# Performance work log

Hardware: AMD Instinct MI355X
Metric: run time of the kernel (lower is better)

## Reference

```python
import jax, jax.numpy as jnp
import numpy as np

T, B, D, H, V = 48, 512, 1024, 1024, 8


def setup_inputs() -> dict:
    key = jax.random.key(0)
    k = jax.random.split(key, 8)
    s = 1.0 / np.sqrt(H)  # torch default LSTM init scale
    return {
        "decoder_hiddens": jax.random.normal(k[0], (T, 1, B, D), dtype=jnp.float32),
        "outputs": jax.random.normal(k[1], (T, B, V), dtype=jnp.float32),
        "captions": jax.random.randint(k[2], (T, B), 0, 10000, dtype=jnp.int64),
        "W_ih": jax.random.uniform(k[3], (4 * H, 2 * D), jnp.float32, -s, s),
        "W_hh": jax.random.uniform(k[4], (4 * H, H), jnp.float32, -s, s),
        "b_ih": jax.random.uniform(k[5], (4 * H,), jnp.float32, -s, s),
        "b_hh": jax.random.uniform(k[6], (4 * H,), jnp.float32, -s, s),
    }


def reference(decoder_hiddens, outputs, captions, W_ih, W_hh, b_ih, b_hh):
    # decoder_hiddens: [T, 1, B, D] -> [T, B, D] (num_layers*dirs flattened into D)
    dh = decoder_hiddens.transpose(0, 2, 1, 3).reshape(T, B, -1)

    # caption mask: tokens != 0 (pad) and != 2 (EOS)
    mask = ((captions != 0) & (captions != 2)).astype(dh.dtype)  # [T, B]
    lens = mask.sum(axis=0)  # [B]
    pooled = (mask[:, :, None] * dh).sum(axis=0) / lens[:, None]  # [B, D]

    # per-step input: cat([decoder_hidden_t, pooled]) for t = 1..T-1
    xs = jnp.concatenate(
        [dh[1:], jnp.broadcast_to(pooled, (T - 1, B, dh.shape[-1]))], axis=-1
    )  # [T-1, B, 2D]

    def lstm_step(carry, x):
        h, c = carry
        gates = x @ W_ih.T + b_ih + h @ W_hh.T + b_hh  # [B, 4H]
        i, f, g, o = jnp.split(gates, 4, axis=-1)  # torch gate order i,f,g,o
        i, f, o = jax.nn.sigmoid(i), jax.nn.sigmoid(f), jax.nn.sigmoid(o)
        c = f * c + i * jnp.tanh(g)
        h = o * jnp.tanh(c)
        return (h, c), h

    h0 = jnp.zeros((B, H), dh.dtype)
    c0 = jnp.zeros((B, H), dh.dtype)
    _, hs = jax.lax.scan(lstm_step, (h0, c0), xs)  # [T-1, B, H]

    # feats_recons[0] stays zero (loop starts at t=1), then transpose to [B, T, H]
    feats = jnp.concatenate([jnp.zeros((1, B, H), dh.dtype), hs], axis=0)
    return feats.transpose(1, 0, 2)
```

## Files before the change

kernel.cpp:

```cpp
#include <hip/hip_runtime.h>
#include <math.h>
#include <stdint.h>

#define B_ 512
#define D_ 1024
#define H_ 1024
#define T_ 48
#define NG 4096

typedef _Float16 half8 __attribute__((ext_vector_type(8)));
typedef float f32x4 __attribute__((ext_vector_type(4)));

#define AG_LOAD(p)      __hip_atomic_load((p), __ATOMIC_RELAXED, __HIP_MEMORY_SCOPE_AGENT)
#define AG_STORE(p, v)  __hip_atomic_store((p), (v), __ATOMIC_RELAXED, __HIP_MEMORY_SCOPE_AGENT)

__device__ __forceinline__ void cp16(const void* g, void* l) {
  __builtin_amdgcn_global_load_lds(
      (__attribute__((address_space(1))) const unsigned int*)(uintptr_t)g,
      (__attribute__((address_space(3))) unsigned int*)(uintptr_t)l, 16, 0, 0);
}

__device__ __forceinline__ float sigmoidf_(float x) { return 1.0f / (1.0f + expf(-x)); }

__device__ __forceinline__ float fast_sig(float x) {
  return __builtin_amdgcn_rcpf(1.0f + __expf(-x));
}
__device__ __forceinline__ float fast_tanh(float x) {
  return 1.0f - 2.0f * __builtin_amdgcn_rcpf(1.0f + __expf(2.0f * x));
}

__global__ void prep_w(const float* __restrict__ W_ih,
                       _Float16* __restrict__ Wx1, _Float16* __restrict__ Wp) {
  int idx = blockIdx.x * 256 + threadIdx.x;
  const int n1 = NG * H_;
  if (idx < n1) {
    int j = idx >> 10, k = idx & 1023;
    Wx1[idx] = (_Float16)W_ih[j * 2048 + k];
  } else {
    int i3 = idx - n1;
    int j = i3 >> 10, k = i3 & 1023;
    Wp[i3] = (_Float16)W_ih[j * 2048 + 1024 + k];
  }
}

__global__ void prep_wfrag(const float* __restrict__ W_hh, _Float16* __restrict__ Wf) {
  int f = blockIdx.x * 256 + threadIdx.x;
  int cb = f >> 13;
  int rem = f & 8191;
  int n = rem >> 11;
  int kc = (rem >> 6) & 31;
  int lane = rem & 63;
  int l16 = lane & 15, quad = lane >> 4;
  const float* s = W_hh + (size_t)(n * 1024 + cb * 16 + l16) * 1024 + kc * 32 + quad * 8;
  half8 v;
#pragma unroll
  for (int i = 0; i < 8; ++i) v[i] = (_Float16)s[i];
  *(half8*)(Wf + (size_t)f * 8) = v;
}

__global__ void pool_conv(const float* __restrict__ dh, const int* __restrict__ caps,
                          _Float16* __restrict__ dh16, _Float16* __restrict__ pooled16) {
  int tid = blockIdx.x * 256 + threadIdx.x;
  int b = tid >> 10;
  float sum = 0.0f, cnt = 0.0f;
  for (int t = 0; t < T_; ++t) {
    int cap = caps[t * B_ + b];
    float v = dh[(size_t)t * (B_ * D_) + tid];
    if (cap != 0 && cap != 2) { sum += v; cnt += 1.0f; }
    if (t >= 1) dh16[(size_t)t * (B_ * D_) + tid] = (_Float16)v;
  }
  pooled16[tid] = (_Float16)(sum / cnt);
}

__global__ void init_zero(float* __restrict__ out, unsigned* __restrict__ bar) {
  int tid = blockIdx.x * 256 + threadIdx.x;
  int b = tid >> 10, d = tid & 1023;
  out[(size_t)b * (T_ * H_) + d] = 0.0f;
  if (tid < 4096) AG_STORE(&bar[tid], 0u);
}

__global__ __launch_bounds__(256) void gemm_pool(
    const _Float16* __restrict__ A, const _Float16* __restrict__ Wp,
    const float* __restrict__ b_ih, const float* __restrict__ b_hh,
    float* __restrict__ Xc) {
  __shared__ __align__(16) _Float16 sA[64 * 32];
  __shared__ __align__(16) _Float16 sB[128 * 32];
  const int tid = threadIdx.x;
  const int wave = tid >> 6, lane = tid & 63;
  const int quad = lane >> 4, l16 = lane & 15;
  const int wm = wave & 1, wn = wave >> 1;
  const int n0 = blockIdx.x * 128;
  const int b0 = blockIdx.y * 64;
  const int rS = tid >> 2, cS = tid & 3;

  f32x4 acc[2][4] = {};
  for (int k0 = 0; k0 < 1024; k0 += 32) {
    cp16(A + (size_t)(b0 + rS) * 1024 + k0 + cS * 8, sA + wave * 512);
    cp16(Wp + (size_t)(n0 + rS) * 1024 + k0 + cS * 8, sB + wave * 512);
    cp16(Wp + (size_t)(n0 + 64 + rS) * 1024 + k0 + cS * 8, sB + 2048 + wave * 512);
    __syncthreads();
    half8 a[2], bfr[4];
#pragma unroll
    for (int m = 0; m < 2; ++m)
      a[m] = *(const half8*)(sA + (wm * 32 + m * 16 + l16) * 32 + quad * 8);
#pragma unroll
    for (int n = 0; n < 4; ++n)
      bfr[n] = *(const half8*)(sB + (wn * 64 + n * 16 + l16) * 32 + quad * 8);
#pragma unroll
    for (int m = 0; m < 2; ++m)
#pragma unroll
      for (int n = 0; n < 4; ++n)
        acc[m][n] = __builtin_amdgcn_mfma_f32_16x16x32_f16(a[m], bfr[n], acc[m][n], 0, 0, 0);
    __syncthreads();
  }
#pragma unroll
  for (int m = 0; m < 2; ++m) {
#pragma unroll
    for (int n = 0; n < 4; ++n) {
      int nn = n0 + wn * 64 + n * 16 + l16;
      float bias = b_ih[nn] + b_hh[nn];
#pragma unroll
      for (int r = 0; r < 4; ++r) {
        int bb = b0 + wm * 32 + m * 16 + quad * 4 + r;
        Xc[(size_t)bb * NG + nn] = acc[m][n][r] + bias;
      }
    }
  }
}

__global__ __launch_bounds__(256) void gemm_x(
    const _Float16* __restrict__ A, const _Float16* __restrict__ Bw,
    const float* __restrict__ Xc, _Float16* __restrict__ Xall) {
  __shared__ __align__(16) _Float16 sA[2][128 * 32];
  __shared__ __align__(16) _Float16 sB[2][128 * 32];
  const int tid = threadIdx.x;
  const int wave = tid >> 6, lane = tid & 63;
  const int quad = lane >> 4, l16 = lane & 15;
  const int wm = wave & 1, wn = wave >> 1;
  const int n0 = blockIdx.x * 128;
  const int m0 = blockIdx.y * 128;
  const int rS = tid >> 2, cS = tid & 3;

  const _Float16* aR0 = A + (size_t)(m0 + rS) * 1024 + cS * 8;
  const _Float16* aR1 = A + (size_t)(m0 + 64 + rS) * 1024 + cS * 8;
  const _Float16* bR0 = Bw + (size_t)(n0 + rS) * 1024 + cS * 8;
  const _Float16* bR1 = Bw + (size_t)(n0 + 64 + rS) * 1024 + cS * 8;

  f32x4 acc[4][4] = {};

  auto stage = [&](int buf, int k0) {
    cp16(aR0 + k0, &sA[buf][wave * 512]);
    cp16(aR1 + k0, &sA[buf][2048 + wave * 512]);
    cp16(bR0 + k0, &sB[buf][wave * 512]);
    cp16(bR1 + k0, &sB[buf][2048 + wave * 512]);
  };
  auto compute = [&](int cur) {
    half8 a[4], b[4];
#pragma unroll
    for (int m = 0; m < 4; ++m)
      a[m] = *(const half8*)&sA[cur][(wm * 64 + m * 16 + l16) * 32 + quad * 8];
#pragma unroll
    for (int n = 0; n < 4; ++n)
      b[n] = *(const half8*)&sB[cur][(wn * 64 + n * 16 + l16) * 32 + quad * 8];
#pragma unroll
    for (int m = 0; m < 4; ++m)
#pragma unroll
      for (int n = 0; n < 4; ++n)
        acc[m][n] = __builtin_amdgcn_mfma_f32_16x16x32_f16(a[m], b[n], acc[m][n], 0, 0, 0);
  };

  stage(0, 0);
  __syncthreads();
  for (int it = 0; it < 31; ++it) {
    const int cur = it & 1;
    stage(cur ^ 1, (it + 1) * 32);
    compute(cur);
    __syncthreads();
  }
  compute(1);

#pragma unroll
  for (int m = 0; m < 4; ++m) {
#pragma unroll
    for (int n = 0; n < 4; ++n) {
      const int col = n0 + wn * 64 + n * 16 + l16;
#pragma unroll
      for (int r = 0; r < 4; ++r) {
        const int row = m0 + wm * 64 + m * 16 + quad * 4 + r;
        Xall[(size_t)row * NG + col] =
            (_Float16)(acc[m][n][r] + Xc[(size_t)(row & 511) * NG + col]);
      }
    }
  }
}

__global__ __launch_bounds__(256, 1) void lstm_all(
    const _Float16* __restrict__ Wf, const _Float16* __restrict__ Xall,
    _Float16* __restrict__ hs, float* __restrict__ out,
    unsigned* __restrict__ bar) {
  __shared__ __align__(16) _Float16 wlds[65536];
  const int tid = threadIdx.x;
  const int wave = tid >> 6, lane = tid & 63;
  const int quad = lane >> 4, l16 = lane & 15;
  const int cb = blockIdx.x >> 2, bb = blockIdx.x & 3;
  const int col = cb * 16 + l16;

  {
    const _Float16* src = Wf + (size_t)cb * 65536;
#pragma unroll
    for (int i = 0; i < 32; ++i)
      cp16(src + (size_t)(i * 256 + wave * 64 + lane) * 8,
           wlds + (i * 256 + wave * 64) * 8);
  }
  __syncthreads();

  float cc[2][4] = {{0.f, 0.f, 0.f, 0.f}, {0.f, 0.f, 0.f, 0.f}};

  _Float16 xh[2][4][4];
  auto prefetchX = [&](int t) {
    const _Float16* xb =
        Xall + ((size_t)(t - 1) * 512 + bb * 128 + wave * 32) * NG + col;
#pragma unroll
    for (int m = 0; m < 2; ++m)
#pragma unroll
      for (int r = 0; r < 4; ++r) {
        const _Float16* xr = xb + (size_t)(m * 16 + quad * 4 + r) * NG;
#pragma unroll
        for (int n = 0; n < 4; ++n) xh[m][n][r] = xr[n * 1024];
      }
  };
  prefetchX(1);

  for (int t = 1; t < T_; ++t) {
    f32x4 acc[2][4] = {};
    if (t > 1) {
      const _Float16* hp = hs + (size_t)(t - 1) * 524288;
      const _Float16* aB0 = hp + (size_t)(bb * 128 + wave * 32 + l16) * 1024 + quad * 8;
      const _Float16* aB1 = aB0 + 16 * 1024;
      half8 abuf[6][2][2];
#define LOADA(P, CH)                                      \
  do {                                                    \
    abuf[P][0][0] = *(const half8*)(aB0 + (CH) * 64);      \
    abuf[P][0][1] = *(const half8*)(aB0 + (CH) * 64 + 32); \
    abuf[P][1][0] = *(const half8*)(aB1 + (CH) * 64);      \
    abuf[P][1][1] = *(const half8*)(aB1 + (CH) * 64 + 32); \
  } while (0)
      LOADA(0, 0);
      LOADA(1, 1);
      LOADA(2, 2);
      LOADA(3, 3);
      LOADA(4, 4);
      LOADA(5, 5);
#pragma unroll
      for (int ch = 0; ch < 16; ++ch) {
        half8 bf[2][4];
#pragma unroll
        for (int kk = 0; kk < 2; ++kk)
#pragma unroll
          for (int n = 0; n < 4; ++n)
            bf[kk][n] =
                *(const half8*)&wlds[(size_t)((n * 32 + ch * 2 + kk) * 64 + lane) * 8];
        const int p = ch % 6;
#pragma unroll
        for (int kk = 0; kk < 2; ++kk)
#pragma unroll
          for (int m = 0; m < 2; ++m)
#pragma unroll
            for (int n = 0; n < 4; ++n)
              acc[m][n] = __builtin_amdgcn_mfma_f32_16x16x32_f16(
                  abuf[p][m][kk], bf[kk][n], acc[m][n], 0, 0, 0);
        if (ch < 10) LOADA(p, ch + 6);
      }
#undef LOADA
    }

    _Float16* hw = hs + (size_t)t * 524288;
#pragma unroll
    for (int m = 0; m < 2; ++m)
#pragma unroll
      for (int r = 0; r < 4; ++r) {
        int b = bb * 128 + wave * 32 + m * 16 + quad * 4 + r;
        float iv = acc[m][0][r] + (float)xh[m][0][r];
        float fv = acc[m][1][r] + (float)xh[m][1][r];
        float gv = acc[m][2][r] + (float)xh[m][2][r];
        float ov = acc[m][3][r] + (float)xh[m][3][r];
        float ig = fast_sig(iv), fg = fast_sig(fv), og = fast_sig(ov);
        float gg = fast_tanh(gv);
        float cn = fg * cc[m][r] + ig * gg;
        cc[m][r] = cn;
        float hv = og * fast_tanh(cn);
        _Float16 hv16 = (_Float16)hv;
        AG_STORE((unsigned short*)(hw + (size_t)b * 1024 + col),
                 __builtin_bit_cast(unsigned short, hv16));
        out[(size_t)b * (T_ * H_) + (size_t)t * H_ + col] = hv;
      }

    if (t + 1 < T_) {
      __syncthreads();
      if (tid == 0)
        AG_STORE(&bar[(bb * 64 + cb) * 16], (unsigned)t);
      prefetchX(t + 1);
      if (tid < 64) {
        const unsigned* f = bar + (bb * 64 + tid) * 16;
        for (int spin = 0; spin < (1 << 20); ++spin) {
          if (AG_LOAD(f) >= (unsigned)t) break;
          __builtin_amdgcn_s_sleep(1);
        }
      }
      __syncthreads();
      __builtin_amdgcn_sched_barrier(0);
    }
  }
}

extern "C" void kernel_launch(void* const* d_in, const int* in_sizes, int n_in,
                              void* d_out, int out_size, void* d_ws, size_t ws_size,
                              hipStream_t stream) {
  (void)in_sizes; (void)n_in; (void)out_size; (void)ws_size;
  const float* dh   = (const float*)d_in[0];
  const int*   caps = (const int*)d_in[2];
  const float* W_ih = (const float*)d_in[3];
  const float* W_hh = (const float*)d_in[4];
  const float* b_ih = (const float*)d_in[5];
  const float* b_hh = (const float*)d_in[6];
  float* out = (float*)d_out;

  char* ws = (char*)d_ws;
  _Float16* Wx116 = (_Float16*)(ws);
  _Float16* Wfrag = (_Float16*)(ws + 8388608);
  _Float16* Wp    = (_Float16*)(ws + 16777216);
  _Float16* dh16  = (_Float16*)(ws + 25165824);
  _Float16* pld16 = (_Float16*)(ws + 75497472);
  float*    Xc    = (float*)   (ws + 76546048);
  _Float16* Xall  = (_Float16*)(ws + 84934656);
  unsigned* bar   = (unsigned*)(ws + 282066944);

  prep_w<<<32768, 256, 0, stream>>>(W_ih, Wx116, Wp);
  prep_wfrag<<<2048, 256, 0, stream>>>(W_hh, Wfrag);
  pool_conv<<<2048, 256, 0, stream>>>(dh, caps, dh16, pld16);
  init_zero<<<2048, 256, 0, stream>>>(out, bar);
  gemm_pool<<<dim3(32, 8), 256, 0, stream>>>(pld16, Wp, b_ih, b_hh, Xc);
  gemm_x<<<dim3(32, 188), 256, 0, stream>>>(dh16 + 524288, Wx116, Xc, Xall);
  lstm_all<<<256, 256, 0, stream>>>(Wfrag, Xall, dh16, out, bar);
}
```

Measured before the change: 1.108 ms.

## Split recurrent K reduction across two wave groups in persistent LSTM kernel

Doubles the persistent LSTM block to 512 threads and splits the per-step h·W_hh reduction in K between two groups of four waves. Each group does half the chunks. Non-owner waves write their partial accumulators to a per-block global scratch buffer, which reuses the Wp workspace. Owner waves add those partials and run the gate math and stores. The aim is to halve the serial MFMA and load chain per wave on the latency-bound critical path of each step, at the cost of an extra block barrier, a global-memory round trip per step, and possible register pressure from the tighter launch bounds.

```diff
diff --git a/kernel.cpp b/kernel.cpp
--- a/kernel.cpp
+++ b/kernel.cpp
@@ -194,23 +194,28 @@
   }
 }
 
-__global__ __launch_bounds__(256, 1) void lstm_all(
+__global__ __launch_bounds__(512, 2) void lstm_all(
     const _Float16* __restrict__ Wf, const _Float16* __restrict__ Xall,
     _Float16* __restrict__ hs, float* __restrict__ out,
-    unsigned* __restrict__ bar) {
+    unsigned* __restrict__ bar, float* __restrict__ xch) {
   __shared__ __align__(16) _Float16 wlds[65536];
   const int tid = threadIdx.x;
   const int wave = tid >> 6, lane = tid & 63;
+  const int grp = wave >> 2;
+  const int wl = wave & 3;
   const int quad = lane >> 4, l16 = lane & 15;
   const int cb = blockIdx.x >> 2, bb = blockIdx.x & 3;
   const int col = cb * 16 + l16;
+  const int kb = grp * 8;
+  const bool owner = (grp == 0) ? (wl < 2) : (wl >= 2);
+  float* xch_b = xch + (size_t)blockIdx.x * 8192;
 
   {
     const _Float16* src = Wf + (size_t)cb * 65536;
 #pragma unroll
-    for (int i = 0; i < 32; ++i)
-      cp16(src + (size_t)(i * 256 + wave * 64 + lane) * 8,
-           wlds + (i * 256 + wave * 64) * 8);
+    for (int i = 0; i < 16; ++i)
+      cp16(src + (size_t)((i * 8 + wave) * 64 + lane) * 8,
+           wlds + ((i * 8 + wave) * 64) * 8);
   }
   __syncthreads();
 
@@ -219,7 +224,7 @@
   _Float16 xh[2][4][4];
   auto prefetchX = [&](int t) {
     const _Float16* xb =
-        Xall + ((size_t)(t - 1) * 512 + bb * 128 + wave * 32) * NG + col;
+        Xall + ((size_t)(t - 1) * 512 + bb * 128 + wl * 32) * NG + col;
 #pragma unroll
     for (int m = 0; m < 2; ++m)
 #pragma unroll
@@ -229,13 +234,13 @@
         for (int n = 0; n < 4; ++n) xh[m][n][r] = xr[n * 1024];
       }
   };
-  prefetchX(1);
+  if (owner) prefetchX(1);
 
   for (int t = 1; t < T_; ++t) {
     f32x4 acc[2][4] = {};
     if (t > 1) {
       const _Float16* hp = hs + (size_t)(t - 1) * 524288;
-      const _Float16* aB0 = hp + (size_t)(bb * 128 + wave * 32 + l16) * 1024 + quad * 8;
+      const _Float16* aB0 = hp + (size_t)(bb * 128 + wl * 32 + l16) * 1024 + quad * 8;
       const _Float16* aB1 = aB0 + 16 * 1024;
       half8 abuf[6][2][2];
 #define LOADA(P, CH)                                      \
@@ -245,21 +250,22 @@
     abuf[P][1][0] = *(const half8*)(aB1 + (CH) * 64);      \
     abuf[P][1][1] = *(const half8*)(aB1 + (CH) * 64 + 32); \
   } while (0)
-      LOADA(0, 0);
-      LOADA(1, 1);
-      LOADA(2, 2);
-      LOADA(3, 3);
-      LOADA(4, 4);
-      LOADA(5, 5);
-#pragma unroll
-      for (int ch = 0; ch < 16; ++ch) {
+      LOADA(0, kb + 0);
+      LOADA(1, kb + 1);
+      LOADA(2, kb + 2);
+      LOADA(3, kb + 3);
+      LOADA(4, kb + 4);
+      LOADA(5, kb + 5);
+#pragma unroll
+      for (int ch = 0; ch < 8; ++ch) {
+        const int cg = kb + ch;
         half8 bf[2][4];
 #pragma unroll
         for (int kk = 0; kk < 2; ++kk)
 #pragma unroll
           for (int n = 0; n < 4; ++n)
             bf[kk][n] =
-                *(const half8*)&wlds[(size_t)((n * 32 + ch * 2 + kk) * 64 + lane) * 8];
+                *(const half8*)&wlds[(size_t)((n * 32 + cg * 2 + kk) * 64 + lane) * 8];
         const int p = ch % 6;
 #pragma unroll
         for (int kk = 0; kk < 2; ++kk)
@@ -269,37 +275,61 @@
             for (int n = 0; n < 4; ++n)
               acc[m][n] = __builtin_amdgcn_mfma_f32_16x16x32_f16(
                   abuf[p][m][kk], bf[kk][n], acc[m][n], 0, 0, 0);
-        if (ch < 10) LOADA(p, ch + 6);
+        if (ch < 2) LOADA(p, kb + ch + 6);
       }
 #undef LOADA
     }
 
-    _Float16* hw = hs + (size_t)t * 524288;
-#pragma unroll
-    for (int m = 0; m < 2; ++m)
-#pragma unroll
-      for (int r = 0; r < 4; ++r) {
-        int b = bb * 128 + wave * 32 + m * 16 + quad * 4 + r;
-        float iv = acc[m][0][r] + (float)xh[m][0][r];
-        float fv = acc[m][1][r] + (float)xh[m][1][r];
-        float gv = acc[m][2][r] + (float)xh[m][2][r];
-        float ov = acc[m][3][r] + (float)xh[m][3][r];
-        float ig = fast_sig(iv), fg = fast_sig(fv), og = fast_sig(ov);
-        float gg = fast_tanh(gv);
-        float cn = fg * cc[m][r] + ig * gg;
-        cc[m][r] = cn;
-        float hv = og * fast_tanh(cn);
-        _Float16 hv16 = (_Float16)hv;
-        AG_STORE((unsigned short*)(hw + (size_t)b * 1024 + col),
-                 __builtin_bit_cast(unsigned short, hv16));
-        out[(size_t)b * (T_ * H_) + (size_t)t * H_ + col] = hv;
-      }
+    if (t > 1 && !owner) {
+#pragma unroll
+      for (int m = 0; m < 2; ++m)
+#pragma unroll
+        for (int n = 0; n < 4; ++n)
+#pragma unroll
+          for (int r = 0; r < 4; ++r)
+            xch_b[(wl * 32 + m * 16 + quad * 4 + r) * 64 + n * 16 + l16] =
+                acc[m][n][r];
+    }
+    __syncthreads();
+    if (owner) {
+      if (t > 1) {
+#pragma unroll
+        for (int m = 0; m < 2; ++m)
+#pragma unroll
+          for (int n = 0; n < 4; ++n)
+#pragma unroll
+            for (int r = 0; r < 4; ++r)
+              acc[m][n][r] +=
+                  xch_b[(wl * 32 + m * 16 + quad * 4 + r) * 64 + n * 16 + l16];
+      }
+
+      _Float16* hw = hs + (size_t)t * 524288;
+#pragma unroll
+      for (int m = 0; m < 2; ++m)
+#pragma unroll
+        for (int r = 0; r < 4; ++r) {
+          int b = bb * 128 + wl * 32 + m * 16 + quad * 4 + r;
+          float iv = acc[m][0][r] + (float)xh[m][0][r];
+          float fv = acc[m][1][r] + (float)xh[m][1][r];
+          float gv = acc[m][2][r] + (float)xh[m][2][r];
+          float ov = acc[m][3][r] + (float)xh[m][3][r];
+          float ig = fast_sig(iv), fg = fast_sig(fv), og = fast_sig(ov);
+          float gg = fast_tanh(gv);
+          float cn = fg * cc[m][r] + ig * gg;
+          cc[m][r] = cn;
+          float hv = og * fast_tanh(cn);
+          _Float16 hv16 = (_Float16)hv;
+          AG_STORE((unsigned short*)(hw + (size_t)b * 1024 + col),
+                   __builtin_bit_cast(unsigned short, hv16));
+          out[(size_t)b * (T_ * H_) + (size_t)t * H_ + col] = hv;
+        }
+    }
 
     if (t + 1 < T_) {
       __syncthreads();
       if (tid == 0)
         AG_STORE(&bar[(bb * 64 + cb) * 16], (unsigned)t);
-      prefetchX(t + 1);
+      if (owner) prefetchX(t + 1);
       if (tid < 64) {
         const unsigned* f = bar + (bb * 64 + tid) * 16;
         for (int spin = 0; spin < (1 << 20); ++spin) {
@@ -341,5 +371,5 @@
   init_zero<<<2048, 256, 0, stream>>>(out, bar);
   gemm_pool<<<dim3(32, 8), 256, 0, stream>>>(pld16, Wp, b_ih, b_hh, Xc);
   gemm_x<<<dim3(32, 188), 256, 0, stream>>>(dh16 + 524288, Wx116, Xc, Xall);
-  lstm_all<<<256, 256, 0, stream>>>(Wfrag, Xall, dh16, out, bar);
-}
+  lstm_all<<<256, 512, 0, stream>>>(Wfrag, Xall, dh16, out, bar, (float*)Wp);
+}
```

Result: faster. 1.042 ms (-6.0%).
